# Kernel optimization log

Hardware: AMD Instinct MI355X
Metric: run time of the kernel (lower is better)

Reference implementation:

```python
import jax, jax.numpy as jnp
import numpy as np

HEAD_SIZE = 64
B, T, C = 8, 2048, 768
NEG_FILL = -99999999999999.0  # exact constant from the source


def setup_inputs() -> dict:
    key = jax.random.key(0)
    kx, kk, kq, kv = jax.random.split(key, 4)
    x = jax.random.normal(kx, (B, T, C), dtype=jnp.float32)
    # Dense(head_size, use_bias=False) kernels, glorot-ish scale
    s = 1.0 / np.sqrt(C)
    Wk = jax.random.normal(kk, (C, HEAD_SIZE), dtype=jnp.float32) * s
    Wq = jax.random.normal(kq, (C, HEAD_SIZE), dtype=jnp.float32) * s
    Wv = jax.random.normal(kv, (C, HEAD_SIZE), dtype=jnp.float32) * s
    return {"x": x, "Wk": Wk, "Wq": Wq, "Wv": Wv}


def reference(x, Wk, Wq, Wv):
    # x: [B, T, C]
    k = jnp.einsum("btc,cd->btd", x, Wk)  # [B, T, D]
    q = jnp.einsum("btc,cd->btd", x, Wq)
    v = jnp.einsum("btc,cd->btd", x, Wv)
    raw_affinity = jnp.einsum("btd,bsd->bts", q, k)  # [B, T, T]
    t = x.shape[1]
    tri = jnp.tril(jnp.ones((t, t), dtype=jnp.float32))
    # faithful to source: multiplicative mask, scale applied AFTER masking
    mask_mult = jnp.where(tri == 1.0, 1.0, NEG_FILL)
    logits = raw_affinity * mask_mult * (HEAD_SIZE ** -0.5)
    attn = jax.nn.softmax(logits, axis=-1)
    out = jnp.einsum("bts,bsd->btd", attn, v)  # [B, T, D]
    return out
```

## Files before the change

### kernel.cpp

```cpp
#include <hip/hip_runtime.h>
#include <math.h>

#define BATCH 8
#define SEQ   2048
#define CDIM  768
#define HDIM  64
#define QROWS 32
#define NSB   (SEQ / 64)
#define MARGIN 1e-2f
#define MASKC (-99999999999999.0 * 0.125)

__global__ __launch_bounds__(256) void qkv_proj_kernel(
    const float* __restrict__ x,
    const float* __restrict__ Wk,
    const float* __restrict__ Wq,
    const float* __restrict__ Wv,
    double* __restrict__ qd,
    double* __restrict__ kd,
    float*  __restrict__ vf,
    unsigned* __restrict__ wcount)
{
    __shared__ float xs[32][36];
    __shared__ float wqs[32 * 64];
    __shared__ float wks[32 * 64];
    __shared__ float wvs[32 * 64];

    const int tid = threadIdx.x;
    if (blockIdx.x == 0 && tid == 0) *wcount = 0u;
    const int tx  = tid & 15;
    const int ty  = tid >> 4;
    const size_t row0 = (size_t)blockIdx.x * 32;

    double qa[2][4] = {{0, 0, 0, 0}, {0, 0, 0, 0}};
    double ka[2][4] = {{0, 0, 0, 0}, {0, 0, 0, 0}};
    float  va[2][4] = {{0, 0, 0, 0}, {0, 0, 0, 0}};

    for (int cc = 0; cc < CDIM; cc += 32) {
        __syncthreads();
        {
            const int r  = tid >> 3;
            const int c4 = tid & 7;
            const float4 v4 = *reinterpret_cast<const float4*>(
                &x[(row0 + r) * CDIM + cc + c4 * 4]);
            *reinterpret_cast<float4*>(&xs[r][c4 * 4]) = v4;
        }
        {
            const float4* wqg = reinterpret_cast<const float4*>(&Wq[(size_t)cc * HDIM]);
            const float4* wkg = reinterpret_cast<const float4*>(&Wk[(size_t)cc * HDIM]);
            const float4* wvg = reinterpret_cast<const float4*>(&Wv[(size_t)cc * HDIM]);
            float4* wql = reinterpret_cast<float4*>(wqs);
            float4* wkl = reinterpret_cast<float4*>(wks);
            float4* wvl = reinterpret_cast<float4*>(wvs);
            #pragma unroll
            for (int it = 0; it < 2; ++it) {
                const int t = tid + it * 256;
                wql[t] = wqg[t];
                wkl[t] = wkg[t];
                wvl[t] = wvg[t];
            }
        }
        __syncthreads();
        #pragma unroll 4
        for (int c = 0; c < 32; ++c) {
            const float4 wq4 = *reinterpret_cast<const float4*>(&wqs[c * 64 + tx * 4]);
            const float4 wk4 = *reinterpret_cast<const float4*>(&wks[c * 64 + tx * 4]);
            const float4 wv4 = *reinterpret_cast<const float4*>(&wvs[c * 64 + tx * 4]);
            #pragma unroll
            for (int i = 0; i < 2; ++i) {
                const float  xv = xs[ty * 2 + i][c];
                const double xd = (double)xv;
                qa[i][0] += xd * (double)wq4.x;
                qa[i][1] += xd * (double)wq4.y;
                qa[i][2] += xd * (double)wq4.z;
                qa[i][3] += xd * (double)wq4.w;
                ka[i][0] += xd * (double)wk4.x;
                ka[i][1] += xd * (double)wk4.y;
                ka[i][2] += xd * (double)wk4.z;
                ka[i][3] += xd * (double)wk4.w;
                va[i][0] += xv * wv4.x;
                va[i][1] += xv * wv4.y;
                va[i][2] += xv * wv4.z;
                va[i][3] += xv * wv4.w;
            }
        }
    }
    #pragma unroll
    for (int i = 0; i < 2; ++i) {
        const size_t row = row0 + ty * 2 + i;
        *reinterpret_cast<double2*>(&qd[row * HDIM + tx * 4])     = make_double2(qa[i][0], qa[i][1]);
        *reinterpret_cast<double2*>(&qd[row * HDIM + tx * 4 + 2]) = make_double2(qa[i][2], qa[i][3]);
        *reinterpret_cast<double2*>(&kd[row * HDIM + tx * 4])     = make_double2(ka[i][0], ka[i][1]);
        *reinterpret_cast<double2*>(&kd[row * HDIM + tx * 4 + 2]) = make_double2(ka[i][2], ka[i][3]);
        *reinterpret_cast<float4*>(&vf[row * HDIM + tx * 4]) =
            make_float4(va[i][0], va[i][1], va[i][2], va[i][3]);
    }
}

__device__ __forceinline__ unsigned long long rowcap_mask(
    float a0, float a1, float a2, float a3,
    int rg, int sb, int tx, unsigned gsh, float& mrun)
{
    a0 = (sb * 64 + tx      > rg) ? a0 : 3.0e38f;
    a1 = (sb * 64 + 16 + tx > rg) ? a1 : 3.0e38f;
    a2 = (sb * 64 + 32 + tx > rg) ? a2 : 3.0e38f;
    a3 = (sb * 64 + 48 + tx > rg) ? a3 : 3.0e38f;
    float tmin = fminf(fminf(a0, a1), fminf(a2, a3));
    #pragma unroll
    for (int off = 8; off > 0; off >>= 1)
        tmin = fminf(tmin, __shfl_xor(tmin, off, 16));
    mrun = fminf(mrun, tmin);
    const float thr = mrun + MARGIN;
    const unsigned long long b0 = __ballot((a0 <= thr) && (a0 < 3.0e37f));
    const unsigned long long b1 = __ballot((a1 <= thr) && (a1 < 3.0e37f));
    const unsigned long long b2 = __ballot((a2 <= thr) && (a2 < 3.0e37f));
    const unsigned long long b3 = __ballot((a3 <= thr) && (a3 < 3.0e37f));
    return ((b0 >> gsh) & 0xFFFFull)
         | (((b1 >> gsh) & 0xFFFFull) << 16)
         | (((b2 >> gsh) & 0xFFFFull) << 32)
         | (((b3 >> gsh) & 0xFFFFull) << 48);
}

#define STAGE(KF, SB)                                                          \
    { const double* ksrc = kd + ((size_t)b * SEQ + (size_t)(SB) * 64) * HDIM;  \
      _Pragma("unroll")                                                        \
      for (int it = 0; it < 8; ++it) {                                         \
          const int r = rb + it * 8;                                           \
          const double2 v2 = *reinterpret_cast<const double2*>(                \
              &ksrc[(size_t)r * HDIM + 2 * c2]);                               \
          KF[r][2 * c2]     = (float)v2.x;                                     \
          KF[r][2 * c2 + 1] = (float)v2.y; } }

#define BODY(KF, SB)                                                           \
    { float s00 = 0.f, s01 = 0.f, s02 = 0.f, s03 = 0.f;                        \
      float s10 = 0.f, s11 = 0.f, s12 = 0.f, s13 = 0.f;                        \
      _Pragma("unroll")                                                        \
      for (int d4 = 0; d4 < 16; ++d4) {                                        \
          const float4 q0 = *reinterpret_cast<const float4*>(&qf[2 * ty][4 * d4]);     \
          const float4 q1 = *reinterpret_cast<const float4*>(&qf[2 * ty + 1][4 * d4]); \
          const float4 k0 = *reinterpret_cast<const float4*>(&KF[tx][4 * d4]);         \
          const float4 k1 = *reinterpret_cast<const float4*>(&KF[16 + tx][4 * d4]);    \
          const float4 k2 = *reinterpret_cast<const float4*>(&KF[32 + tx][4 * d4]);    \
          const float4 k3 = *reinterpret_cast<const float4*>(&KF[48 + tx][4 * d4]);    \
          s00 += q0.x*k0.x + q0.y*k0.y + q0.z*k0.z + q0.w*k0.w;                \
          s01 += q0.x*k1.x + q0.y*k1.y + q0.z*k1.z + q0.w*k1.w;                \
          s02 += q0.x*k2.x + q0.y*k2.y + q0.z*k2.z + q0.w*k2.w;                \
          s03 += q0.x*k3.x + q0.y*k3.y + q0.z*k3.z + q0.w*k3.w;                \
          s10 += q1.x*k0.x + q1.y*k0.y + q1.z*k0.z + q1.w*k0.w;                \
          s11 += q1.x*k1.x + q1.y*k1.y + q1.z*k1.z + q1.w*k1.w;                \
          s12 += q1.x*k2.x + q1.y*k2.y + q1.z*k2.z + q1.w*k2.w;                \
          s13 += q1.x*k3.x + q1.y*k3.y + q1.z*k3.z + q1.w*k3.w;                \
      }                                                                        \
      const unsigned long long m0 =                                            \
          rowcap_mask(s00, s01, s02, s03, r0 + 2 * ty,     (SB), tx, gsh, mrun0); \
      const unsigned long long m1 =                                            \
          rowcap_mask(s10, s11, s12, s13, r0 + 2 * ty + 1, (SB), tx, gsh, mrun1); \
      if (tx == 0) {                                                           \
          candmask[2 * ty][(SB)]     = m0;                                     \
          candmask[2 * ty + 1][(SB)] = m1; } }

__global__ __launch_bounds__(256) void argmin_kernel(
    const double* __restrict__ qd,
    const double* __restrict__ kd,
    const float*  __restrict__ vf,
    float* __restrict__ out,
    unsigned* __restrict__ wcount,
    unsigned* __restrict__ wlist)
{
    __shared__ float qf[QROWS][68];
    __shared__ float kfA[64][68];
    __shared__ float kfB[64][68];
    __shared__ unsigned long long candmask[QROWS][NSB];

    const int tid  = threadIdx.x;
    const int lane = tid & 63;
    const unsigned gsh = (unsigned)(lane & 48);
    const int tx  = tid & 15;
    const int ty  = tid >> 4;
    const int b   = blockIdx.x;
    const int byy = blockIdx.y;
    const int tb  = (byy < 32) ? byy : 95 - byy;
    const int r0  = tb * QROWS;
    const int sb0 = tb >> 1;

    {
        const double* qsrc = qd + ((size_t)b * SEQ + r0) * HDIM;
        #pragma unroll
        for (int it = 0; it < 8; ++it) {
            const int idx = tid + it * 256;
            qf[idx >> 6][idx & 63] = (float)qsrc[(idx >> 6) * HDIM + (idx & 63)];
        }
    }

    const int c2 = tid & 31;
    const int rb = tid >> 5;

    float mrun0 = 3.0e38f, mrun1 = 3.0e38f;

    STAGE(kfA, sb0);
    __syncthreads();

    int sb = sb0;
    while (true) {
        if (sb + 1 < NSB) STAGE(kfB, sb + 1);
        BODY(kfA, sb);
        __syncthreads();
        ++sb;
        if (sb >= NSB) break;
        if (sb + 1 < NSB) STAGE(kfA, sb + 1);
        BODY(kfB, sb);
        __syncthreads();
        ++sb;
        if (sb >= NSB) break;
    }
    __syncthreads();

    const int row = tid >> 3, l8 = tid & 7;
    const int rg  = r0 + row;
    int n = 0;
    double min1 = 1.0e300, min2 = 1.0e300;
    int amin = -1;
    const double* qrow = qd + ((size_t)b * SEQ + rg) * HDIM;
    for (int sbi = sb0; sbi < NSB; ++sbi) {
        unsigned long long m = candmask[row][sbi];
        while (m) {
            const int p = __ffsll((long long)m) - 1;
            m &= m - 1;
            const int col = sbi * 64 + p;
            if (col <= rg) continue;
            ++n;
            const double* krow = kd + ((size_t)b * SEQ + col) * HDIM;
            double part = 0.0;
            #pragma unroll
            for (int dd = 0; dd < 8; ++dd)
                part += qrow[8 * l8 + dd] * krow[8 * l8 + dd];
            #pragma unroll
            for (int off = 4; off > 0; off >>= 1)
                part += __shfl_xor(part, off, 8);
            if (part < min1) { min2 = min1; min1 = part; amin = col; }
            else if (part < min2) { min2 = part; }
        }
    }
    const bool flag = (n == 0) || (min1 > -1e-10) || ((min2 - min1) < 1e-11);
    float* orow = out + ((size_t)b * SEQ + rg) * HDIM;
    if (flag) {
        if (l8 == 0) {
            const unsigned slot = atomicAdd(wcount, 1u);
            wlist[slot] = ((unsigned)b << 16) | (unsigned)rg;
        }
    } else {
        const float* vrow = vf + ((size_t)b * SEQ + amin) * HDIM;
        const float4 v0 = *reinterpret_cast<const float4*>(&vrow[8 * l8]);
        const float4 v1 = *reinterpret_cast<const float4*>(&vrow[8 * l8 + 4]);
        *reinterpret_cast<float4*>(&orow[8 * l8])     = v0;
        *reinterpret_cast<float4*>(&orow[8 * l8 + 4]) = v1;
    }
}

__global__ __launch_bounds__(256) void exact_kernel(
    const double* __restrict__ qd,
    const double* __restrict__ kd,
    const float*  __restrict__ vf,
    float* __restrict__ out,
    const unsigned* __restrict__ wcount,
    const unsigned* __restrict__ wlist)
{
    __shared__ double qs[HDIM];
    __shared__ double lgbuf[SEQ];
    __shared__ float  pbuf[SEQ];
    __shared__ float  outacc[4][HDIM];
    __shared__ double mred[4];
    __shared__ float  psred[4];

    const int tid  = threadIdx.x;
    const int wid  = tid >> 6, lane = tid & 63;
    const unsigned nflag = *wcount;

    for (unsigned i = blockIdx.x; i < nflag; i += gridDim.x) {
        const unsigned e = wlist[i];
        const int b  = (int)(e >> 16);
        const int rg = (int)(e & 0xFFFFu);
        float* orow = out + ((size_t)b * SEQ + rg) * HDIM;

        if (tid < HDIM) qs[tid] = qd[((size_t)b * SEQ + rg) * HDIM + tid];
        __syncthreads();

        const double qv = qs[lane];
        const double* kb = kd + (size_t)b * SEQ * HDIM;
        const int cbase = 512 * wid;

        for (int cc = 0; cc < 512; cc += 4) {
            const int c = cbase + cc;
            double p0 = kb[(size_t)(c + 0) * HDIM + lane] * qv;
            double p1 = kb[(size_t)(c + 1) * HDIM + lane] * qv;
            double p2 = kb[(size_t)(c + 2) * HDIM + lane] * qv;
            double p3 = kb[(size_t)(c + 3) * HDIM + lane] * qv;
            #pragma unroll
            for (int off = 32; off > 0; off >>= 1) {
                p0 += __shfl_xor(p0, off, 64);
                p1 += __shfl_xor(p1, off, 64);
                p2 += __shfl_xor(p2, off, 64);
                p3 += __shfl_xor(p3, off, 64);
            }
            if (lane == 0) {
                lgbuf[c]     = p0 * ((c     <= rg) ? 0.125 : MASKC);
                lgbuf[c + 1] = p1 * ((c + 1 <= rg) ? 0.125 : MASKC);
                lgbuf[c + 2] = p2 * ((c + 2 <= rg) ? 0.125 : MASKC);
                lgbuf[c + 3] = p3 * ((c + 3 <= rg) ? 0.125 : MASKC);
            }
        }
        __syncthreads();

        double mymax = -1.0e300;
        #pragma unroll
        for (int it = 0; it < 8; ++it)
            mymax = fmax(mymax, lgbuf[tid + it * 256]);
        #pragma unroll
        for (int off = 32; off > 0; off >>= 1)
            mymax = fmax(mymax, __shfl_xor(mymax, off, 64));
        if (lane == 0) mred[wid] = mymax;
        __syncthreads();
        const double M = fmax(fmax(mred[0], mred[1]), fmax(mred[2], mred[3]));

        float mypsum = 0.f;
        #pragma unroll
        for (int it = 0; it < 8; ++it) {
            const int col = tid + it * 256;
            const double dl = lgbuf[col] - M;
            const float p = (dl < -80.0) ? 0.f : (float)exp(dl);
            pbuf[col] = p;
            mypsum += p;
        }
        #pragma unroll
        for (int off = 32; off > 0; off >>= 1)
            mypsum += __shfl_xor(mypsum, off, 64);
        if (lane == 0) psred[wid] = mypsum;
        __syncthreads();
        const float PS = psred[0] + psred[1] + psred[2] + psred[3];

        const int d = tid & 63, chunk = tid >> 6;
        float acc = 0.f;
        for (int cc = 0; cc < 512; ++cc) {
            const int col = chunk * 512 + cc;
            acc += pbuf[col] * vf[((size_t)b * SEQ + col) * HDIM + d];
        }
        outacc[chunk][d] = acc;
        __syncthreads();
        if (tid < HDIM)
            orow[tid] = (outacc[0][tid] + outacc[1][tid] +
                         outacc[2][tid] + outacc[3][tid]) / PS;
        __syncthreads();
    }
}

extern "C" void kernel_launch(void* const* d_in, const int* in_sizes, int n_in,
                              void* d_out, int out_size, void* d_ws, size_t ws_size,
                              hipStream_t stream)
{
    const float* x  = (const float*)d_in[0];
    const float* Wk = (const float*)d_in[1];
    const float* Wq = (const float*)d_in[2];
    const float* Wv = (const float*)d_in[3];
    float* out = (float*)d_out;

    double* qd = (double*)d_ws;
    double* kd = qd + (size_t)BATCH * SEQ * HDIM;
    float*  vf = (float*)(kd + (size_t)BATCH * SEQ * HDIM);
    unsigned* wcount = (unsigned*)(vf + (size_t)BATCH * SEQ * HDIM);
    unsigned* wlist  = wcount + 16;

    qkv_proj_kernel<<<dim3(512), dim3(256), 0, stream>>>(x, Wk, Wq, Wv, qd, kd, vf, wcount);
    argmin_kernel<<<dim3(8, 64), dim3(256), 0, stream>>>(qd, kd, vf, out, wcount, wlist);
    exact_kernel<<<dim3(128), dim3(256), 0, stream>>>(qd, kd, vf, out, wcount, wlist);
}
```

Before: 342.5 us.

## Double-buffer QKV projection tiles with async global-to-LDS loads

The QKV projection kernel now stages x and weight tiles straight into shared memory with global_load_lds and double-buffers them. The next 64-wide chunk is prefetched while the current one is computed, and the K-chunk grows from 32 to 64. The goal is to hide global load latency and halve the number of barriers. In exchange, LDS use roughly triples, which may cut occupancy. Correctness also depends on the async loads having completed before the barrier, and there is no explicit vmcnt wait.

After: 360.6 us. 1.05x slower.

```diff
diff --git a/kernel.cpp b/kernel.cpp
--- a/kernel.cpp
+++ b/kernel.cpp
@@ -9,6 +9,10 @@
 #define NSB   (SEQ / 64)
 #define MARGIN 1e-2f
 #define MASKC (-99999999999999.0 * 0.125)
+
+#define GLL(GP, LP) __builtin_amdgcn_global_load_lds(                          \
+    (const __attribute__((address_space(1))) void*)(GP),                       \
+    (__attribute__((address_space(3))) void*)(LP), 16, 0, 0)
 
 __global__ __launch_bounds__(256) void qkv_proj_kernel(
     const float* __restrict__ x,
@@ -20,10 +24,10 @@
     float*  __restrict__ vf,
     unsigned* __restrict__ wcount)
 {
-    __shared__ float xs[32][36];
-    __shared__ float wqs[32 * 64];
-    __shared__ float wks[32 * 64];
-    __shared__ float wvs[32 * 64];
+    __shared__ __align__(16) float xs[2][32][64];
+    __shared__ __align__(16) float wqs[2][64 * 64];
+    __shared__ __align__(16) float wks[2][64 * 64];
+    __shared__ __align__(16) float wvs[2][64 * 64];
 
     const int tid = threadIdx.x;
     if (blockIdx.x == 0 && tid == 0) *wcount = 0u;
@@ -35,39 +39,42 @@
     double ka[2][4] = {{0, 0, 0, 0}, {0, 0, 0, 0}};
     float  va[2][4] = {{0, 0, 0, 0}, {0, 0, 0, 0}};
 
-    for (int cc = 0; cc < CDIM; cc += 32) {
-        __syncthreads();
-        {
-            const int r  = tid >> 3;
-            const int c4 = tid & 7;
-            const float4 v4 = *reinterpret_cast<const float4*>(
-                &x[(row0 + r) * CDIM + cc + c4 * 4]);
-            *reinterpret_cast<float4*>(&xs[r][c4 * 4]) = v4;
-        }
-        {
-            const float4* wqg = reinterpret_cast<const float4*>(&Wq[(size_t)cc * HDIM]);
-            const float4* wkg = reinterpret_cast<const float4*>(&Wk[(size_t)cc * HDIM]);
-            const float4* wvg = reinterpret_cast<const float4*>(&Wv[(size_t)cc * HDIM]);
-            float4* wql = reinterpret_cast<float4*>(wqs);
-            float4* wkl = reinterpret_cast<float4*>(wks);
-            float4* wvl = reinterpret_cast<float4*>(wvs);
-            #pragma unroll
-            for (int it = 0; it < 2; ++it) {
-                const int t = tid + it * 256;
-                wql[t] = wqg[t];
-                wkl[t] = wkg[t];
-                wvl[t] = wvg[t];
-            }
-        }
-        __syncthreads();
+#define ISSUE(BUF, CC) do {                                                    \
+    const int wb = (tid & 192);              \
+    _Pragma("unroll")                                                          \
+    for (int it = 0; it < 2; ++it) {                                           \
+        const int t = tid + it * 256;               \
+        GLL(&x[(row0 + (t >> 4)) * CDIM + (CC) + (t & 15) * 4],                \
+            &xs[BUF][0][0] + (size_t)(it * 256 + wb) * 4);                     \
+    }                                                                          \
+    const float4* wqg = reinterpret_cast<const float4*>(&Wq[(size_t)(CC) * HDIM]); \
+    const float4* wkg = reinterpret_cast<const float4*>(&Wk[(size_t)(CC) * HDIM]); \
+    const float4* wvg = reinterpret_cast<const float4*>(&Wv[(size_t)(CC) * HDIM]); \
+    _Pragma("unroll")                                                          \
+    for (int it = 0; it < 4; ++it) {                                           \
+        const int t  = tid + it * 256;             \
+        const int lb = (it * 256 + wb) * 4;                                    \
+        GLL(wqg + t, &wqs[BUF][0] + lb);                                       \
+        GLL(wkg + t, &wks[BUF][0] + lb);                                       \
+        GLL(wvg + t, &wvs[BUF][0] + lb);                                       \
+    }                                                                          \
+} while (0)
+
+    ISSUE(0, 0);
+    __syncthreads();
+
+    int buf = 0;
+    for (int cc = 0; cc < CDIM; cc += 64) {
+        if (cc + 64 < CDIM) ISSUE(buf ^ 1, cc + 64);
+
         #pragma unroll 4
-        for (int c = 0; c < 32; ++c) {
-            const float4 wq4 = *reinterpret_cast<const float4*>(&wqs[c * 64 + tx * 4]);
-            const float4 wk4 = *reinterpret_cast<const float4*>(&wks[c * 64 + tx * 4]);
-            const float4 wv4 = *reinterpret_cast<const float4*>(&wvs[c * 64 + tx * 4]);
+        for (int c = 0; c < 64; ++c) {
+            const float4 wq4 = *reinterpret_cast<const float4*>(&wqs[buf][c * 64 + tx * 4]);
+            const float4 wk4 = *reinterpret_cast<const float4*>(&wks[buf][c * 64 + tx * 4]);
+            const float4 wv4 = *reinterpret_cast<const float4*>(&wvs[buf][c * 64 + tx * 4]);
             #pragma unroll
             for (int i = 0; i < 2; ++i) {
-                const float  xv = xs[ty * 2 + i][c];
+                const float  xv = xs[buf][2 * ty + i][c];
                 const double xd = (double)xv;
                 qa[i][0] += xd * (double)wq4.x;
                 qa[i][1] += xd * (double)wq4.y;
@@ -83,7 +90,10 @@
                 va[i][3] += xv * wv4.w;
             }
         }
-    }
+        __syncthreads();
+        buf ^= 1;
+    }
+
     #pragma unroll
     for (int i = 0; i < 2; ++i) {
         const size_t row = row0 + ty * 2 + i;
@@ -94,6 +104,7 @@
         *reinterpret_cast<float4*>(&vf[row * HDIM + tx * 4]) =
             make_float4(va[i][0], va[i][1], va[i][2], va[i][3]);
     }
+#undef ISSUE
 }
 
 __device__ __forceinline__ unsigned long long rowcap_mask(
```
